# Optimization experiments

Measured on AMD Instinct MI355X. Metric: run time of the kernel, lower is better.

Reference implementation:

```python
import jax, jax.numpy as jnp
import numpy as np

N_NODES = 50000
N_EDGES = 800000
IN_DIM = 256
HIDDEN = 32
HEADS = 4
OUT_DIM = 64


def setup_inputs() -> dict:
    key = jax.random.key(0)
    k1, k2, k3, k4, k5, k6, k7 = jax.random.split(key, 7)
    h = jax.random.normal(k1, (N_NODES, IN_DIM), dtype=jnp.float32)
    src = jax.random.randint(k2, (N_EDGES,), 0, N_NODES, dtype=jnp.int32)
    dst = jax.random.randint(k3, (N_EDGES,), 0, N_NODES, dtype=jnp.int32)
    # xavier_normal with relu gain, per-head weights
    gain = float(np.sqrt(2.0))
    W1 = gain * jnp.sqrt(2.0 / (IN_DIM + HIDDEN)) * jax.random.normal(k4, (HEADS, IN_DIM, HIDDEN), dtype=jnp.float32)
    a1 = gain * jnp.sqrt(2.0 / (2 * HIDDEN + 1)) * jax.random.normal(k5, (HEADS, 2 * HIDDEN), dtype=jnp.float32)
    W2 = gain * jnp.sqrt(2.0 / (HIDDEN * HEADS + OUT_DIM)) * jax.random.normal(k6, (1, HIDDEN * HEADS, OUT_DIM), dtype=jnp.float32)
    a2 = gain * jnp.sqrt(2.0 / (2 * OUT_DIM + 1)) * jax.random.normal(k7, (1, 2 * OUT_DIM), dtype=jnp.float32)
    return {"h": h, "src": src, "dst": dst, "W1": W1, "a1": a1, "W2": W2, "a2": a2}


def _gat_layer(x, src, dst, W, a):
    # x: [N, in], W: [H, in, d], a: [H, 2d]
    N = x.shape[0]
    d = W.shape[-1]
    z = jnp.einsum('ni,hio->nho', x, W)                    # [N, H, d]
    a_s, a_d = a[:, :d], a[:, d:]
    es = jnp.einsum('nho,ho->nh', z, a_s)                  # per-node src score
    ed = jnp.einsum('nho,ho->nh', z, a_d)                  # per-node dst score
    e = jax.nn.leaky_relu(es[src] + ed[dst])               # [E, H]
    # segment (per-destination) softmax over incoming edges
    emax = jax.ops.segment_max(e, dst, num_segments=N)     # [N, H]
    ex = jnp.exp(e - emax[dst])
    denom = jax.ops.segment_sum(ex, dst, num_segments=N)   # [N, H]
    alpha = ex / denom[dst]                                # [E, H]
    # scatter weighted sum of source feats back to destinations
    out = jax.ops.segment_sum(alpha[:, :, None] * z[src], dst, num_segments=N)  # [N, H, d]
    return out.reshape(N, -1)


def reference(h, src, dst, W1, a1, W2, a2):
    h1 = jax.nn.elu(_gat_layer(h, src, dst, W1, a1))       # [N, HEADS*HIDDEN]
    return _gat_layer(h1, src, dst, W2, a2)                # [N, OUT_DIM]
```

## Files before the change

kernel.cpp:

```cpp
#include <hip/hip_runtime.h>
#include <hip/hip_bf16.h>
#include <math.h>

#define N_NODES 50000
#define N_EDGES 800000
#define IN_DIM 256
#define HID 32
#define HEADS 4
#define OUT_DIM 64

#define SCAN_CHUNK 1024
#define SCAN_BLOCKS ((N_NODES + SCAN_CHUNK - 1) / SCAN_CHUNK)

typedef __attribute__((ext_vector_type(8))) short bf16x8;
typedef __attribute__((ext_vector_type(4))) float f32x4;

__device__ __forceinline__ float lrelu(float e) { return e > 0.f ? e : 0.01f * e; }
__device__ __forceinline__ float bflo(unsigned u) { return __uint_as_float(u << 16); }
__device__ __forceinline__ float bfhi(unsigned u) { return __uint_as_float(u & 0xffff0000u); }

__device__ __forceinline__ unsigned short rne_bf16(float x) {
    unsigned u = __float_as_uint(x);
    unsigned r = u + 0x7fffu + ((u >> 16) & 1u);
    return (unsigned short)(r >> 16);
}

__device__ __forceinline__ void splitf(float x, short& hi, short& lo) {
    unsigned u = __float_as_uint(x);
    unsigned short h = (unsigned short)(u >> 16);
    float hf = __uint_as_float(((unsigned)h) << 16);
    float l = x - hf;
    unsigned short lb = (unsigned short)(__float_as_uint(l) >> 16);
    hi = (short)h;
    lo = (short)lb;
}


__global__ void __launch_bounds__(256) prep_kernel(
        const float* __restrict__ W1, const float* __restrict__ a1,
        const float* __restrict__ W2, const float* __restrict__ a2,
        unsigned short* __restrict__ B1h, unsigned short* __restrict__ B1l,
        unsigned short* __restrict__ B2h, unsigned short* __restrict__ B2l,
        int* __restrict__ count) {
    int gid = blockIdx.x * 256 + threadIdx.x;
    if (gid < N_NODES) count[gid] = 0;

    int k = blockIdx.x;
    int c = threadIdx.x;
    if (c < 144) {
        float val = 0.f;
        if (c < 128) {
            val = W1[(size_t)(c >> 5) * IN_DIM * HID + (size_t)k * HID + (c & 31)];
        } else if (c < 136) {
            int j = c - 128;
            int hd = (j < 4) ? j : (j - 4);
            int off = (j < 4) ? 0 : HID;
            const float* Wp = W1 + (size_t)hd * IN_DIM * HID + (size_t)k * HID;
            const float* ap = a1 + hd * 2 * HID + off;
            float s = 0.f;
            for (int o = 0; o < HID; o++) s += Wp[o] * ap[o];
            val = s;
        }
        unsigned short hi = rne_bf16(val);
        float hf = __uint_as_float(((unsigned)hi) << 16);
        unsigned short lo = rne_bf16(val - hf);
        int s_ = k >> 5, q = (k >> 3) & 3, j8 = k & 7;
        int nt = c >> 4, L = q * 16 + (c & 15);
        size_t idx = (((size_t)s_ * 9 + nt) * 64 + L) * 8 + j8;
        B1h[idx] = hi;
        B1l[idx] = lo;
    } else if (c >= 160 && c < 240 && k < 128) {
        int c2 = c - 160;
        float val = 0.f;
        if (c2 < 64) {
            val = W2[(size_t)k * OUT_DIM + c2];
        } else if (c2 < 66) {
            const float* ap = a2 + (c2 - 64) * OUT_DIM;
            const float* Wp = W2 + (size_t)k * OUT_DIM;
            float s = 0.f;
            for (int o = 0; o < OUT_DIM; o++) s += Wp[o] * ap[o];
            val = s;
        }
        unsigned short hi = rne_bf16(val);
        float hf = __uint_as_float(((unsigned)hi) << 16);
        unsigned short lo = rne_bf16(val - hf);
        int s_ = k >> 5, q = (k >> 3) & 3, j8 = k & 7;
        int nt = c2 >> 4, L = q * 16 + (c2 & 15);
        size_t idx = (((size_t)s_ * 5 + nt) * 64 + L) * 8 + j8;
        B2h[idx] = hi;
        B2l[idx] = lo;
    }
}


__global__ void hist_kernel(const int* __restrict__ dst, int* __restrict__ count,
                            int* __restrict__ rank) {
    int i = blockIdx.x * blockDim.x + threadIdx.x;
    if (i < N_EDGES) rank[i] = atomicAdd(&count[dst[i]], 1);
}

__global__ void scan1_kernel(const int* __restrict__ count, int* __restrict__ row_start,
                             int* __restrict__ blocksum) {
    __shared__ int sdata[256];
    int t = threadIdx.x;
    int base = blockIdx.x * SCAN_CHUNK + t * 4;
    int v[4];
    int s = 0;
#pragma unroll
    for (int j = 0; j < 4; j++) {
        int idx = base + j;
        int x = (idx < N_NODES) ? count[idx] : 0;
        v[j] = x;
        s += x;
    }
    sdata[t] = s;
    __syncthreads();
    for (int off = 1; off < 256; off <<= 1) {
        int u = (t >= off) ? sdata[t - off] : 0;
        __syncthreads();
        sdata[t] += u;
        __syncthreads();
    }
    int excl = sdata[t] - s;
#pragma unroll
    for (int j = 0; j < 4; j++) {
        int idx = base + j;
        if (idx < N_NODES) row_start[idx] = excl;
        excl += v[j];
    }
    if (t == 255) blocksum[blockIdx.x] = sdata[255];
}

__global__ void scan23_kernel(int* __restrict__ row_start, const int* __restrict__ blocksum) {
    __shared__ int pre;
    int t = threadIdx.x;
    if (t < 64) {
        int v = (t < SCAN_BLOCKS) ? blocksum[t] : 0;
#pragma unroll
        for (int off = 1; off < 64; off <<= 1) {
            int u = __shfl_up(v, off);
            if (t >= off) v += u;
        }
        if (t == blockIdx.x) pre = v - blocksum[t];
    }
    __syncthreads();
    int add = pre;
    int base = blockIdx.x * SCAN_CHUNK + t * 4;
#pragma unroll
    for (int j = 0; j < 4; j++) {
        int idx = base + j;
        if (idx < N_NODES) row_start[idx] += add;
    }
}

__global__ void scatter_kernel(const int* __restrict__ src, const int* __restrict__ dst,
                               const int* __restrict__ rank, const int* __restrict__ row_start,
                               int* __restrict__ esrc, int* __restrict__ edst) {
    int i = blockIdx.x * blockDim.x + threadIdx.x;
    if (i < N_EDGES) {
        int d = dst[i];
        int pos = row_start[d] + rank[i];
        esrc[pos] = src[i];
        edst[pos] = d;
    }
}


__global__ void __launch_bounds__(256) proj1_mfma(
        const float* __restrict__ h, const unsigned short* __restrict__ Bh,
        const unsigned short* __restrict__ Bl, __hip_bfloat16* __restrict__ z1b,
        float* __restrict__ es1, float* __restrict__ ed1) {
    int tid = threadIdx.x;
    int wave = tid >> 6;
    int L = tid & 63;
    int q = L >> 4, L15 = L & 15;
    int n0 = blockIdx.x * 64 + wave * 16;

    int rowA = n0 + L15;
    int rrA = rowA < N_NODES ? rowA : N_NODES - 1;
    const float* hrow = h + (size_t)rrA * IN_DIM + q * 8;

    f32x4 acc[9];
#pragma unroll
    for (int nt = 0; nt < 9; nt++) acc[nt] = (f32x4)(0.f);

    float4 x0 = *(const float4*)(hrow);
    float4 x1 = *(const float4*)(hrow + 4);

#pragma unroll
    for (int s = 0; s < 8; s++) {
        int sn = (s < 7) ? s + 1 : 7;
        float4 p0 = *(const float4*)(hrow + sn * 32);
        float4 p1 = *(const float4*)(hrow + sn * 32 + 4);

        float xs[8] = {x0.x, x0.y, x0.z, x0.w, x1.x, x1.y, x1.z, x1.w};
        bf16x8 ah, al;
#pragma unroll
        for (int j = 0; j < 8; j++) {
            short hi, lo;
            splitf(xs[j], hi, lo);
            ah[j] = hi;
            al[j] = lo;
        }

        const bf16x8* bhp = (const bf16x8*)(Bh + ((size_t)s * 9 * 64) * 8 + (size_t)L * 8);
        const bf16x8* blp = (const bf16x8*)(Bl + ((size_t)s * 9 * 64) * 8 + (size_t)L * 8);
#pragma unroll
        for (int nt = 0; nt < 9; nt++) {
            bf16x8 bh = bhp[nt * 64];
            acc[nt] = __builtin_amdgcn_mfma_f32_16x16x32_bf16(ah, bh, acc[nt], 0, 0, 0);
            acc[nt] = __builtin_amdgcn_mfma_f32_16x16x32_bf16(al, bh, acc[nt], 0, 0, 0);
        }
        {
            bf16x8 bl8 = blp[8 * 64];
            acc[8] = __builtin_amdgcn_mfma_f32_16x16x32_bf16(ah, bl8, acc[8], 0, 0, 0);
        }
        x0 = p0;
        x1 = p1;
    }

#pragma unroll
    for (int r = 0; r < 4; r++) {
        int rowc = n0 + q * 4 + r;
        if (rowc < N_NODES) {
#pragma unroll
            for (int nt = 0; nt < 8; nt++)
                z1b[(size_t)rowc * 128 + nt * 16 + L15] = __float2bfloat16(acc[nt][r]);
            if (L15 < 4) es1[rowc * HEADS + L15] = acc[8][r];
            else if (L15 < 8) ed1[rowc * HEADS + (L15 - 4)] = acc[8][r];
        }
    }
}


__global__ void edge1_p(const int* __restrict__ esrc, const int* __restrict__ edst,
                        const float* __restrict__ es1, const float* __restrict__ ed1,
                        float* __restrict__ p1) {
    int pos = blockIdx.x * 256 + threadIdx.x;
    if (pos >= N_EDGES) return;
    int s = esrc[pos], d = edst[pos];
    float4 es = *(const float4*)(es1 + 4 * (size_t)s);
    float4 ed = *(const float4*)(ed1 + 4 * (size_t)d);
    p1[0 * (size_t)N_EDGES + pos] = __expf(lrelu(es.x + ed.x));
    p1[1 * (size_t)N_EDGES + pos] = __expf(lrelu(es.y + ed.y));
    p1[2 * (size_t)N_EDGES + pos] = __expf(lrelu(es.z + ed.z));
    p1[3 * (size_t)N_EDGES + pos] = __expf(lrelu(es.w + ed.w));
}

__global__ void edge2_p(const int* __restrict__ esrc, const int* __restrict__ edst,
                        const float* __restrict__ es2, const float* __restrict__ ed2,
                        float* __restrict__ p2) {
    int pos = blockIdx.x * 256 + threadIdx.x;
    if (pos >= N_EDGES) return;
    p2[pos] = __expf(lrelu(es2[esrc[pos]] + ed2[edst[pos]]));
}


__global__ void __launch_bounds__(256) agg1_kernel(
        const __hip_bfloat16* __restrict__ z1b, const float* __restrict__ p1,
        const int* __restrict__ row_start, const int* __restrict__ count,
        const int* __restrict__ esrc, __hip_bfloat16* __restrict__ h1b) {
    int v = blockIdx.x * 4 + (threadIdx.x >> 6);
    int L = threadIdx.x & 63;
    int sub = L >> 4;
    int c16 = L & 15;
    int hd = c16 >> 2;
    int beg = row_start[v], deg = count[v];
    const float* ph = p1 + (size_t)hd * N_EDGES + beg;
    const int* ep = esrc + beg;
    float lacc = 0.f;
    float acc[8];
#pragma unroll
    for (int i = 0; i < 8; i++) acc[i] = 0.f;
    const uint4* zq = (const uint4*)z1b;

    for (int j0 = 0; j0 < deg; j0 += 32) {
        int se[8];
        float q[8];
        uint4 u[8];
#pragma unroll
        for (int g = 0; g < 8; g++) {
            if (j0 + g * 4 < deg) {
                int e = j0 + g * 4 + sub;
                bool val = e < deg;
                int idx = val ? e : 0;
                se[g] = ep[idx];
                float qq = ph[idx];
                q[g] = val ? qq : 0.f;
            }
        }
#pragma unroll
        for (int g = 0; g < 8; g++)
            if (j0 + g * 4 < deg) u[g] = zq[(size_t)se[g] * 16 + c16];
#pragma unroll
        for (int g = 0; g < 8; g++) {
            if (j0 + g * 4 < deg) {
                lacc += q[g];
                acc[0] = fmaf(q[g], bflo(u[g].x), acc[0]);
                acc[1] = fmaf(q[g], bfhi(u[g].x), acc[1]);
                acc[2] = fmaf(q[g], bflo(u[g].y), acc[2]);
                acc[3] = fmaf(q[g], bfhi(u[g].y), acc[3]);
                acc[4] = fmaf(q[g], bflo(u[g].z), acc[4]);
                acc[5] = fmaf(q[g], bfhi(u[g].z), acc[5]);
                acc[6] = fmaf(q[g], bflo(u[g].w), acc[6]);
                acc[7] = fmaf(q[g], bfhi(u[g].w), acc[7]);
            }
        }
    }
    lacc += __shfl_xor(lacc, 1);
    lacc += __shfl_xor(lacc, 2);
    lacc += __shfl_xor(lacc, 16);
    lacc += __shfl_xor(lacc, 32);
    lacc *= 0.25f;
#pragma unroll
    for (int i = 0; i < 8; i++) {
        acc[i] += __shfl_xor(acc[i], 16);
        acc[i] += __shfl_xor(acc[i], 32);
    }
    if (L < 16) {
        float inv = (deg > 0) ? 1.f / lacc : 0.f;
        unsigned w[4];
#pragma unroll
        for (int i = 0; i < 4; i++) {
            float r0 = acc[2 * i] * inv;
            float r1 = acc[2 * i + 1] * inv;
            r0 = r0 > 0.f ? r0 : __expf(r0) - 1.f;
            r1 = r1 > 0.f ? r1 : __expf(r1) - 1.f;
            w[i] = (unsigned)rne_bf16(r0) | ((unsigned)rne_bf16(r1) << 16);
        }
        uint4* dst = (uint4*)(h1b + (size_t)v * 128 + c16 * 8);
        *dst = make_uint4(w[0], w[1], w[2], w[3]);
    }
}


__global__ void __launch_bounds__(256) proj2_mfma(
        const __hip_bfloat16* __restrict__ h1b, const unsigned short* __restrict__ Bh,
        const unsigned short* __restrict__ Bl, __hip_bfloat16* __restrict__ z2b,
        float* __restrict__ es2, float* __restrict__ ed2) {
    int tid = threadIdx.x;
    int wave = tid >> 6;
    int L = tid & 63;
    int q = L >> 4, L15 = L & 15;
    int n0 = blockIdx.x * 64 + wave * 16;

    int rowA = n0 + L15;
    int rrA = rowA < N_NODES ? rowA : N_NODES - 1;
    const bf16x8* hq = (const bf16x8*)(h1b + (size_t)rrA * 128);

    f32x4 acc[5];
#pragma unroll
    for (int nt = 0; nt < 5; nt++) acc[nt] = (f32x4)(0.f);

#pragma unroll
    for (int s = 0; s < 4; s++) {
        bf16x8 a = hq[s * 4 + q];
        const bf16x8* bhp = (const bf16x8*)(Bh + ((size_t)s * 5 * 64) * 8 + (size_t)L * 8);
        const bf16x8* blp = (const bf16x8*)(Bl + ((size_t)s * 5 * 64) * 8 + (size_t)L * 8);
#pragma unroll
        for (int nt = 0; nt < 5; nt++)
            acc[nt] = __builtin_amdgcn_mfma_f32_16x16x32_bf16(a, bhp[nt * 64], acc[nt], 0, 0, 0);
        acc[4] = __builtin_amdgcn_mfma_f32_16x16x32_bf16(a, blp[4 * 64], acc[4], 0, 0, 0);
    }

#pragma unroll
    for (int r = 0; r < 4; r++) {
        int rowc = n0 + q * 4 + r;
        if (rowc < N_NODES) {
#pragma unroll
            for (int nt = 0; nt < 4; nt++)
                z2b[(size_t)rowc * OUT_DIM + nt * 16 + L15] = __float2bfloat16(acc[nt][r]);
            if (L15 == 0) es2[rowc] = acc[4][r];
            else if (L15 == 1) ed2[rowc] = acc[4][r];
        }
    }
}


__global__ void __launch_bounds__(256) agg2_kernel(
        const __hip_bfloat16* __restrict__ z2b, const float* __restrict__ p2,
        const int* __restrict__ row_start, const int* __restrict__ count,
        const int* __restrict__ esrc, float* __restrict__ out) {
    int v = blockIdx.x * 4 + (threadIdx.x >> 6);
    int L = threadIdx.x & 63;
    int sub = L >> 3;
    int c8 = L & 7;
    int beg = row_start[v], deg = count[v];
    const float* ph = p2 + beg;
    const int* ep = esrc + beg;
    float lacc = 0.f;
    float acc[8];
#pragma unroll
    for (int i = 0; i < 8; i++) acc[i] = 0.f;
    const uint4* zq = (const uint4*)z2b;

    for (int j0 = 0; j0 < deg; j0 += 32) {
        int se[4];
        float q[4];
        uint4 u[4];
#pragma unroll
        for (int g = 0; g < 4; g++) {
            if (j0 + g * 8 < deg) {
                int e = j0 + g * 8 + sub;
                bool val = e < deg;
                int idx = val ? e : 0;
                se[g] = ep[idx];
                float qq = ph[idx];
                q[g] = val ? qq : 0.f;
            }
        }
#pragma unroll
        for (int g = 0; g < 4; g++)
            if (j0 + g * 8 < deg) u[g] = zq[(size_t)se[g] * 8 + c8];
#pragma unroll
        for (int g = 0; g < 4; g++) {
            if (j0 + g * 8 < deg) {
                lacc += q[g];
                acc[0] = fmaf(q[g], bflo(u[g].x), acc[0]);
                acc[1] = fmaf(q[g], bfhi(u[g].x), acc[1]);
                acc[2] = fmaf(q[g], bflo(u[g].y), acc[2]);
                acc[3] = fmaf(q[g], bfhi(u[g].y), acc[3]);
                acc[4] = fmaf(q[g], bflo(u[g].z), acc[4]);
                acc[5] = fmaf(q[g], bfhi(u[g].z), acc[5]);
                acc[6] = fmaf(q[g], bflo(u[g].w), acc[6]);
                acc[7] = fmaf(q[g], bfhi(u[g].w), acc[7]);
            }
        }
    }
    lacc += __shfl_xor(lacc, 8);
    lacc += __shfl_xor(lacc, 16);
    lacc += __shfl_xor(lacc, 32);
#pragma unroll
    for (int i = 0; i < 8; i++) {
        acc[i] += __shfl_xor(acc[i], 8);
        acc[i] += __shfl_xor(acc[i], 16);
        acc[i] += __shfl_xor(acc[i], 32);
    }
    if (L < 8) {
        float inv = (deg > 0) ? 1.f / lacc : 0.f;
        float4 r0, r1;
#pragma unroll
        for (int i = 0; i < 8; i++) {
            float r = acc[i] * inv;
            if (i < 4) (&r0.x)[i] = r;
            else (&r1.x)[i - 4] = r;
        }
        float* dst = out + (size_t)v * OUT_DIM + c8 * 8;
        *(float4*)dst = r0;
        *(float4*)(dst + 4) = r1;
    }
}


extern "C" void kernel_launch(void* const* d_in, const int* in_sizes, int n_in,
                              void* d_out, int out_size, void* d_ws, size_t ws_size,
                              hipStream_t stream) {
    const float* h  = (const float*)d_in[0];
    const int* src  = (const int*)d_in[1];
    const int* dst  = (const int*)d_in[2];
    const float* W1 = (const float*)d_in[3];
    const float* a1 = (const float*)d_in[4];
    const float* W2 = (const float*)d_in[5];
    const float* a2 = (const float*)d_in[6];
    float* out = (float*)d_out;

    char* w = (char*)d_ws;
    size_t off = 0;
    auto alloc = [&](size_t bytes) {
        void* p = w + off;
        off = (off + bytes + 255) & ~(size_t)255;
        return p;
    };
    __hip_bfloat16* z1b = (__hip_bfloat16*)alloc((size_t)N_NODES * 128 * 2);
    float* es1 = (float*)alloc((size_t)N_NODES * HEADS * 4);
    float* ed1 = (float*)alloc((size_t)N_NODES * HEADS * 4);
    __hip_bfloat16* h1b = (__hip_bfloat16*)alloc((size_t)N_NODES * 128 * 2);
    __hip_bfloat16* z2b = (__hip_bfloat16*)alloc((size_t)N_NODES * OUT_DIM * 2);
    float* es2 = (float*)alloc((size_t)N_NODES * 4);
    float* ed2 = (float*)alloc((size_t)N_NODES * 4);
    int* count     = (int*)alloc((size_t)N_NODES * 4);
    int* row_start = (int*)alloc((size_t)N_NODES * 4);
    int* rank      = (int*)alloc((size_t)N_EDGES * 4);
    int* blocksum  = (int*)alloc((size_t)SCAN_BLOCKS * 4);
    int* esrc      = (int*)alloc((size_t)N_EDGES * 4);
    int* edst      = (int*)alloc((size_t)N_EDGES * 4);
    float* p1      = (float*)alloc((size_t)N_EDGES * HEADS * 4);
    float* p2      = (float*)alloc((size_t)N_EDGES * 4);
    unsigned short* Bf1h = (unsigned short*)alloc((size_t)8 * 9 * 64 * 8 * 2);
    unsigned short* Bf1l = (unsigned short*)alloc((size_t)8 * 9 * 64 * 8 * 2);
    unsigned short* Bf2h = (unsigned short*)alloc((size_t)4 * 5 * 64 * 8 * 2);
    unsigned short* Bf2l = (unsigned short*)alloc((size_t)4 * 5 * 64 * 8 * 2);

    prep_kernel<<<256, 256, 0, stream>>>(W1, a1, W2, a2, Bf1h, Bf1l, Bf2h, Bf2l, count);
    hist_kernel<<<(N_EDGES + 255) / 256, 256, 0, stream>>>(dst, count, rank);
    scan1_kernel<<<SCAN_BLOCKS, 256, 0, stream>>>(count, row_start, blocksum);
    scan23_kernel<<<SCAN_BLOCKS, 256, 0, stream>>>(row_start, blocksum);
    scatter_kernel<<<(N_EDGES + 255) / 256, 256, 0, stream>>>(src, dst, rank, row_start, esrc, edst);

    const int MBLK = (N_NODES + 63) / 64;
    proj1_mfma<<<MBLK, 256, 0, stream>>>(h, Bf1h, Bf1l, z1b, es1, ed1);
    edge1_p<<<(N_EDGES + 255) / 256, 256, 0, stream>>>(esrc, edst, es1, ed1, p1);
    agg1_kernel<<<N_NODES / 4, 256, 0, stream>>>(z1b, p1, row_start, count, esrc, h1b);
    proj2_mfma<<<MBLK, 256, 0, stream>>>(h1b, Bf2h, Bf2l, z2b, es2, ed2);
    edge2_p<<<(N_EDGES + 255) / 256, 256, 0, stream>>>(esrc, edst, es2, ed2, p2);
    agg2_kernel<<<N_NODES / 4, 256, 0, stream>>>(z2b, p2, row_start, count, esrc, out);
}
```

Baseline: 268.3 us.

## Fuse edge score exponentials into aggregation kernels and drop edst/p buffers

Removes the separate edge1_p/edge2_p kernels that materialised per-edge exp scores into global buffers. The aggregation kernels now gather the source node's score next to its feature row and compute exp(leaky_relu(es+ed)) inline, with the destination score loaded once per node. This also lets the scatter kernel stop writing the sorted edst array. It saves two launches and the write-then-read of the p arrays. In exchange, each aggregation lane repeats the exp work and does an extra small random gather of es per edge.

```diff
diff --git a/kernel.cpp b/kernel.cpp
--- a/kernel.cpp
+++ b/kernel.cpp
@@ -155,14 +155,9 @@
 
 __global__ void scatter_kernel(const int* __restrict__ src, const int* __restrict__ dst,
                                const int* __restrict__ rank, const int* __restrict__ row_start,
-                               int* __restrict__ esrc, int* __restrict__ edst) {
+                               int* __restrict__ esrc) {
     int i = blockIdx.x * blockDim.x + threadIdx.x;
-    if (i < N_EDGES) {
-        int d = dst[i];
-        int pos = row_start[d] + rank[i];
-        esrc[pos] = src[i];
-        edst[pos] = d;
-    }
+    if (i < N_EDGES) esrc[row_start[dst[i]] + rank[i]] = src[i];
 }
 
 
@@ -233,40 +228,18 @@
 }
 
 
-__global__ void edge1_p(const int* __restrict__ esrc, const int* __restrict__ edst,
-                        const float* __restrict__ es1, const float* __restrict__ ed1,
-                        float* __restrict__ p1) {
-    int pos = blockIdx.x * 256 + threadIdx.x;
-    if (pos >= N_EDGES) return;
-    int s = esrc[pos], d = edst[pos];
-    float4 es = *(const float4*)(es1 + 4 * (size_t)s);
-    float4 ed = *(const float4*)(ed1 + 4 * (size_t)d);
-    p1[0 * (size_t)N_EDGES + pos] = __expf(lrelu(es.x + ed.x));
-    p1[1 * (size_t)N_EDGES + pos] = __expf(lrelu(es.y + ed.y));
-    p1[2 * (size_t)N_EDGES + pos] = __expf(lrelu(es.z + ed.z));
-    p1[3 * (size_t)N_EDGES + pos] = __expf(lrelu(es.w + ed.w));
-}
-
-__global__ void edge2_p(const int* __restrict__ esrc, const int* __restrict__ edst,
-                        const float* __restrict__ es2, const float* __restrict__ ed2,
-                        float* __restrict__ p2) {
-    int pos = blockIdx.x * 256 + threadIdx.x;
-    if (pos >= N_EDGES) return;
-    p2[pos] = __expf(lrelu(es2[esrc[pos]] + ed2[edst[pos]]));
-}
-
-
 __global__ void __launch_bounds__(256) agg1_kernel(
-        const __hip_bfloat16* __restrict__ z1b, const float* __restrict__ p1,
-        const int* __restrict__ row_start, const int* __restrict__ count,
-        const int* __restrict__ esrc, __hip_bfloat16* __restrict__ h1b) {
+        const __hip_bfloat16* __restrict__ z1b, const float* __restrict__ es1,
+        const float* __restrict__ ed1, const int* __restrict__ row_start,
+        const int* __restrict__ count, const int* __restrict__ esrc,
+        __hip_bfloat16* __restrict__ h1b) {
     int v = blockIdx.x * 4 + (threadIdx.x >> 6);
     int L = threadIdx.x & 63;
     int sub = L >> 4;
     int c16 = L & 15;
     int hd = c16 >> 2;
     int beg = row_start[v], deg = count[v];
-    const float* ph = p1 + (size_t)hd * N_EDGES + beg;
+    float edv = ed1[v * HEADS + hd];
     const int* ep = esrc + beg;
     float lacc = 0.f;
     float acc[8];
@@ -276,34 +249,36 @@
 
     for (int j0 = 0; j0 < deg; j0 += 32) {
         int se[8];
-        float q[8];
         uint4 u[8];
+        float ev[8];
 #pragma unroll
         for (int g = 0; g < 8; g++) {
             if (j0 + g * 4 < deg) {
                 int e = j0 + g * 4 + sub;
-                bool val = e < deg;
-                int idx = val ? e : 0;
-                se[g] = ep[idx];
-                float qq = ph[idx];
-                q[g] = val ? qq : 0.f;
-            }
-        }
-#pragma unroll
-        for (int g = 0; g < 8; g++)
-            if (j0 + g * 4 < deg) u[g] = zq[(size_t)se[g] * 16 + c16];
+                se[g] = ep[(e < deg) ? e : 0];
+            }
+        }
 #pragma unroll
         for (int g = 0; g < 8; g++) {
             if (j0 + g * 4 < deg) {
-                lacc += q[g];
-                acc[0] = fmaf(q[g], bflo(u[g].x), acc[0]);
-                acc[1] = fmaf(q[g], bfhi(u[g].x), acc[1]);
-                acc[2] = fmaf(q[g], bflo(u[g].y), acc[2]);
-                acc[3] = fmaf(q[g], bfhi(u[g].y), acc[3]);
-                acc[4] = fmaf(q[g], bflo(u[g].z), acc[4]);
-                acc[5] = fmaf(q[g], bfhi(u[g].z), acc[5]);
-                acc[6] = fmaf(q[g], bflo(u[g].w), acc[6]);
-                acc[7] = fmaf(q[g], bfhi(u[g].w), acc[7]);
+                u[g] = zq[(size_t)se[g] * 16 + c16];
+                ev[g] = es1[se[g] * HEADS + hd];
+            }
+        }
+#pragma unroll
+        for (int g = 0; g < 8; g++) {
+            if (j0 + g * 4 < deg) {
+                bool val = (j0 + g * 4 + sub) < deg;
+                float q = val ? __expf(lrelu(ev[g] + edv)) : 0.f;
+                lacc += q;
+                acc[0] = fmaf(q, bflo(u[g].x), acc[0]);
+                acc[1] = fmaf(q, bfhi(u[g].x), acc[1]);
+                acc[2] = fmaf(q, bflo(u[g].y), acc[2]);
+                acc[3] = fmaf(q, bfhi(u[g].y), acc[3]);
+                acc[4] = fmaf(q, bflo(u[g].z), acc[4]);
+                acc[5] = fmaf(q, bfhi(u[g].z), acc[5]);
+                acc[6] = fmaf(q, bflo(u[g].w), acc[6]);
+                acc[7] = fmaf(q, bfhi(u[g].w), acc[7]);
             }
         }
     }
@@ -378,15 +353,16 @@
 
 
 __global__ void __launch_bounds__(256) agg2_kernel(
-        const __hip_bfloat16* __restrict__ z2b, const float* __restrict__ p2,
-        const int* __restrict__ row_start, const int* __restrict__ count,
-        const int* __restrict__ esrc, float* __restrict__ out) {
+        const __hip_bfloat16* __restrict__ z2b, const float* __restrict__ es2,
+        const float* __restrict__ ed2, const int* __restrict__ row_start,
+        const int* __restrict__ count, const int* __restrict__ esrc,
+        float* __restrict__ out) {
     int v = blockIdx.x * 4 + (threadIdx.x >> 6);
     int L = threadIdx.x & 63;
     int sub = L >> 3;
     int c8 = L & 7;
     int beg = row_start[v], deg = count[v];
-    const float* ph = p2 + beg;
+    float edv = ed2[v];
     const int* ep = esrc + beg;
     float lacc = 0.f;
     float acc[8];
@@ -396,34 +372,36 @@
 
     for (int j0 = 0; j0 < deg; j0 += 32) {
         int se[4];
-        float q[4];
         uint4 u[4];
+        float ev[4];
 #pragma unroll
         for (int g = 0; g < 4; g++) {
             if (j0 + g * 8 < deg) {
                 int e = j0 + g * 8 + sub;
-                bool val = e < deg;
-                int idx = val ? e : 0;
-                se[g] = ep[idx];
-                float qq = ph[idx];
-                q[g] = val ? qq : 0.f;
-            }
-        }
-#pragma unroll
-        for (int g = 0; g < 4; g++)
-            if (j0 + g * 8 < deg) u[g] = zq[(size_t)se[g] * 8 + c8];
+                se[g] = ep[(e < deg) ? e : 0];
+            }
+        }
 #pragma unroll
         for (int g = 0; g < 4; g++) {
             if (j0 + g * 8 < deg) {
-                lacc += q[g];
-                acc[0] = fmaf(q[g], bflo(u[g].x), acc[0]);
-                acc[1] = fmaf(q[g], bfhi(u[g].x), acc[1]);
-                acc[2] = fmaf(q[g], bflo(u[g].y), acc[2]);
-                acc[3] = fmaf(q[g], bfhi(u[g].y), acc[3]);
-                acc[4] = fmaf(q[g], bflo(u[g].z), acc[4]);
-                acc[5] = fmaf(q[g], bfhi(u[g].z), acc[5]);
-                acc[6] = fmaf(q[g], bflo(u[g].w), acc[6]);
-                acc[7] = fmaf(q[g], bfhi(u[g].w), acc[7]);
+                u[g] = zq[(size_t)se[g] * 8 + c8];
+                ev[g] = es2[se[g]];
+            }
+        }
+#pragma unroll
+        for (int g = 0; g < 4; g++) {
+            if (j0 + g * 8 < deg) {
+                bool val = (j0 + g * 8 + sub) < deg;
+                float q = val ? __expf(lrelu(ev[g] + edv)) : 0.f;
+                lacc += q;
+                acc[0] = fmaf(q, bflo(u[g].x), acc[0]);
+                acc[1] = fmaf(q, bfhi(u[g].x), acc[1]);
+                acc[2] = fmaf(q, bflo(u[g].y), acc[2]);
+                acc[3] = fmaf(q, bfhi(u[g].y), acc[3]);
+                acc[4] = fmaf(q, bflo(u[g].z), acc[4]);
+                acc[5] = fmaf(q, bfhi(u[g].z), acc[5]);
+                acc[6] = fmaf(q, bflo(u[g].w), acc[6]);
+                acc[7] = fmaf(q, bfhi(u[g].w), acc[7]);
             }
         }
     }
@@ -483,9 +461,6 @@
     int* rank      = (int*)alloc((size_t)N_EDGES * 4);
     int* blocksum  = (int*)alloc((size_t)SCAN_BLOCKS * 4);
     int* esrc      = (int*)alloc((size_t)N_EDGES * 4);
-    int* edst      = (int*)alloc((size_t)N_EDGES * 4);
-    float* p1      = (float*)alloc((size_t)N_EDGES * HEADS * 4);
-    float* p2      = (float*)alloc((size_t)N_EDGES * 4);
     unsigned short* Bf1h = (unsigned short*)alloc((size_t)8 * 9 * 64 * 8 * 2);
     unsigned short* Bf1l = (unsigned short*)alloc((size_t)8 * 9 * 64 * 8 * 2);
     unsigned short* Bf2h = (unsigned short*)alloc((size_t)4 * 5 * 64 * 8 * 2);
@@ -495,13 +470,11 @@
     hist_kernel<<<(N_EDGES + 255) / 256, 256, 0, stream>>>(dst, count, rank);
     scan1_kernel<<<SCAN_BLOCKS, 256, 0, stream>>>(count, row_start, blocksum);
     scan23_kernel<<<SCAN_BLOCKS, 256, 0, stream>>>(row_start, blocksum);
-    scatter_kernel<<<(N_EDGES + 255) / 256, 256, 0, stream>>>(src, dst, rank, row_start, esrc, edst);
+    scatter_kernel<<<(N_EDGES + 255) / 256, 256, 0, stream>>>(src, dst, rank, row_start, esrc);
 
     const int MBLK = (N_NODES + 63) / 64;
     proj1_mfma<<<MBLK, 256, 0, stream>>>(h, Bf1h, Bf1l, z1b, es1, ed1);
-    edge1_p<<<(N_EDGES + 255) / 256, 256, 0, stream>>>(esrc, edst, es1, ed1, p1);
-    agg1_kernel<<<N_NODES / 4, 256, 0, stream>>>(z1b, p1, row_start, count, esrc, h1b);
+    agg1_kernel<<<N_NODES / 4, 256, 0, stream>>>(z1b, es1, ed1, row_start, count, esrc, h1b);
     proj2_mfma<<<MBLK, 256, 0, stream>>>(h1b, Bf2h, Bf2l, z2b, es2, ed2);
-    edge2_p<<<(N_EDGES + 255) / 256, 256, 0, stream>>>(esrc, edst, es2, ed2, p2);
-    agg2_kernel<<<N_NODES / 4, 256, 0, stream>>>(z2b, p2, row_start, count, esrc, out);
-}
+    agg2_kernel<<<N_NODES / 4, 256, 0, stream>>>(z2b, es2, ed2, row_start, count, esrc, out);
+}
```

Result: faster. 230.0 us (-14.3%).
